# Optimization experiments

Hardware: AMD Instinct MI355X
Metric: run time of the kernel (lower is better)

The kernel has to match this reference:

```python
import jax, jax.numpy as jnp
import numpy as np

DROPOUT_RATE = 0.6


def dropout(x, key, rate=DROPOUT_RATE):
    keep = jax.random.bernoulli(key, 1.0 - rate, x.shape)
    return jnp.where(keep, x / (1.0 - rate), 0.0).astype(x.dtype)


def gcn_conv(x, W, b, src, dst, n_nodes):
    # h = x @ W  (tiny linear), then symmetric-normalized scatter-add over edges
    h = x @ W                                             # [N, C_out]
    deg = jax.ops.segment_sum(jnp.ones_like(dst, dtype=h.dtype), dst,
                              num_segments=n_nodes)       # in-degree at targets
    dinv = jnp.where(deg > 0, jax.lax.rsqrt(jnp.maximum(deg, 1.0)), 0.0)
    norm = dinv[src] * dinv[dst]                          # [E]
    msg = h[src] * norm[:, None]                          # [E, C_out] gather
    out = jax.ops.segment_sum(msg, dst, num_segments=n_nodes)  # scatter-add
    return out + b


def setup_inputs() -> dict:
    key = jax.random.key(0)
    k_x, k_e, k_w1, k_w2 = jax.random.split(key, 4)
    N, E = 100000, 6400000
    x = jax.random.normal(k_x, (N, 1), dtype=jnp.float32)
    edge_index = jax.random.randint(k_e, (2, E), 0, N, dtype=jnp.int64)
    # GCNConv weights (glorot-ish scale) and zero biases
    W1 = jax.random.normal(k_w1, (1, 16), dtype=jnp.float32) * (1.0 / np.sqrt(1.0))
    b1 = jnp.zeros((16,), dtype=jnp.float32)
    W2 = jax.random.normal(k_w2, (16, 1), dtype=jnp.float32) * (1.0 / np.sqrt(16.0))
    b2 = jnp.zeros((1,), dtype=jnp.float32)
    return {"x": x, "edge_index": edge_index, "W1": W1, "b1": b1, "W2": W2, "b2": b2}


def reference(x, edge_index, W1, b1, W2, b2):
    n_nodes = x.shape[0]
    src, dst = edge_index[0], edge_index[1]
    k1, k2 = jax.random.split(jax.random.key(42), 2)
    h = dropout(x, k1)
    h = gcn_conv(h, W1, b1, src, dst, n_nodes)
    h = jax.nn.relu(h)
    h = dropout(h, k2)
    out = gcn_conv(h, W2, b2, src, dst, n_nodes)
    return out
```

## Files before the change

### kernel.cpp

```cpp
#include <hip/hip_runtime.h>
#include <hip/hip_bf16.h>
#include <stdint.h>


#define KEEP_P 0.4f
#define RANGE 2048
#define SHIFT 11
#define MASK 2047
#define BPC 512
#define KS 32
#define SEGS (BPC / KS)
#define NBMAX 64
#define TILE 2048
#define TILE4 (TILE / 4)

__host__ __device__ inline unsigned rotl32(unsigned v, int s) {
  return (v << s) | (v >> (32 - s));
}

__host__ __device__ inline void threefry2x32(unsigned key0, unsigned key1,
                                             unsigned x0, unsigned x1,
                                             unsigned& o0, unsigned& o1) {
  unsigned ks0 = key0, ks1 = key1, ks2 = key0 ^ key1 ^ 0x1BD11BDAu;
  unsigned v0 = x0 + ks0, v1 = x1 + ks1;
#define TF_R(r) { v0 += v1; v1 = rotl32(v1, r); v1 ^= v0; }
  TF_R(13) TF_R(15) TF_R(26) TF_R(6)
  v0 += ks1; v1 += ks2 + 1u;
  TF_R(17) TF_R(29) TF_R(16) TF_R(24)
  v0 += ks2; v1 += ks0 + 2u;
  TF_R(13) TF_R(15) TF_R(26) TF_R(6)
  v0 += ks0; v1 += ks1 + 3u;
  TF_R(17) TF_R(29) TF_R(16) TF_R(24)
  v0 += ks1; v1 += ks2 + 4u;
  TF_R(13) TF_R(15) TF_R(26) TF_R(6)
  v0 += ks2; v1 += ks0 + 5u;
#undef TF_R
  o0 = v0; o1 = v1;
}

__device__ inline float u01_from_bits(unsigned bits) {
  return __uint_as_float((bits >> 9) | 0x3f800000u) - 1.0f;
}

__global__ __launch_bounds__(256) void k_part(
    const int* __restrict__ src, const int* __restrict__ dst,
    unsigned* __restrict__ slots, unsigned* __restrict__ cnt,
    int NB, int CAP, int e4, int E) {
  __shared__ unsigned hist[NBMAX], scan_s[NBMAX + 1], off[NBMAX];
  __shared__ unsigned tbase[NBMAX], cur[NBMAX];
  __shared__ unsigned stage[TILE];
  __shared__ unsigned char stage_p[TILE];
  const int tid = threadIdx.x;
  const size_t blkbase = (size_t)blockIdx.x * NB;
  unsigned* myslots = slots + blkbase * CAP;
  for (int p = tid; p < NB; p += 256) cur[p] = (unsigned)(p * CAP);
  const int chunk = (e4 + BPC - 1) / BPC;
  const int j0 = blockIdx.x * chunk;
  const int j1 = min(j0 + chunk, e4);
  const int4* dst4 = reinterpret_cast<const int4*>(dst);
  const int4* src4 = reinterpret_cast<const int4*>(src);

  for (int t0 = j0; t0 < j1; t0 += TILE4) {
    __syncthreads();
    for (int p = tid; p < NB; p += 256) hist[p] = 0u;
    __syncthreads();
    const int ja = t0 + tid, jb = t0 + TILE4 / 2 + tid;
    const bool va = ja < j1 && tid < TILE4 / 2;
    const bool vb = jb < j1;
    int4 da, db;
    if (va) {
      da = dst4[ja];
      atomicAdd(&hist[(unsigned)da.x >> SHIFT], 1u);
      atomicAdd(&hist[(unsigned)da.y >> SHIFT], 1u);
      atomicAdd(&hist[(unsigned)da.z >> SHIFT], 1u);
      atomicAdd(&hist[(unsigned)da.w >> SHIFT], 1u);
    }
    if (vb) {
      db = dst4[jb];
      atomicAdd(&hist[(unsigned)db.x >> SHIFT], 1u);
      atomicAdd(&hist[(unsigned)db.y >> SHIFT], 1u);
      atomicAdd(&hist[(unsigned)db.z >> SHIFT], 1u);
      atomicAdd(&hist[(unsigned)db.w >> SHIFT], 1u);
    }
    __syncthreads();
    if (tid == 0) {
      unsigned acc = 0;
      for (int p = 0; p < NB; ++p) { scan_s[p] = acc; acc += hist[p]; }
      scan_s[NB] = acc;
    }
    __syncthreads();
    for (int p = tid; p < NB; p += 256) {
      off[p] = scan_s[p];
      tbase[p] = cur[p];
      cur[p] += hist[p];
    }
    __syncthreads();
#define STAGE1(d, s) { unsigned ud = (unsigned)(d), us = (unsigned)(s); \
    unsigned p = ud >> SHIFT; unsigned pos = atomicAdd(&off[p], 1u); \
    stage[pos] = (ud & MASK) | (us << SHIFT); stage_p[pos] = (unsigned char)p; }
    if (va) {
      int4 sa = src4[ja];
      STAGE1(da.x, sa.x) STAGE1(da.y, sa.y) STAGE1(da.z, sa.z) STAGE1(da.w, sa.w)
    }
    if (vb) {
      int4 sb = src4[jb];
      STAGE1(db.x, sb.x) STAGE1(db.y, sb.y) STAGE1(db.z, sb.z) STAGE1(db.w, sb.w)
    }
#undef STAGE1
    __syncthreads();
    const int tc = (int)scan_s[NB];
    for (int i = tid; i < tc; i += 256) {
      unsigned p = stage_p[i];
      myslots[tbase[p] + ((unsigned)i - scan_s[p])] = stage[i];
    }
  }
  __syncthreads();
  if (blockIdx.x == 0) {
    for (int t = e4 * 4 + tid; t < E; t += 256) {
      unsigned ud = (unsigned)dst[t], us = (unsigned)src[t];
      unsigned p = ud >> SHIFT;
      unsigned pos = atomicAdd(&cur[p], 1u);
      myslots[pos] = (ud & MASK) | (us << SHIFT);
    }
  }
  __syncthreads();
  for (int p = tid; p < NB; p += 256)
    cnt[blkbase + p] = cur[p] - (unsigned)(p * CAP);
}

__global__ __launch_bounds__(256) void k_deg2(
    const unsigned* __restrict__ slots, const unsigned* __restrict__ cnt,
    unsigned short* __restrict__ part16, int NB, int CAP) {
  __shared__ unsigned bins[RANGE / 2];
  const int tid = threadIdx.x, w = tid >> 6, lane = tid & 63;
  const int p = blockIdx.y, kd = blockIdx.x;
  for (int i = tid; i < RANGE / 2; i += 256) bins[i] = 0u;
  __syncthreads();
  const int b0 = kd * SEGS + w;
  int l[4]; const unsigned* e[4];
#pragma unroll
  for (int s = 0; s < 4; ++s) {
    const int b = b0 + 4 * s;
    l[s] = cnt[(size_t)b * NB + p];
    e[s] = slots + ((size_t)b * NB + p) * CAP;
  }
  const int base1 = 4 * lane, base2 = base1 + 256;
  uint4 u[8]; bool f[8];
#pragma unroll
  for (int s = 0; s < 4; ++s) {
    f[2 * s]     = base1 + 4 <= l[s];
    f[2 * s + 1] = base2 + 4 <= l[s];
    if (f[2 * s])     u[2 * s]     = *reinterpret_cast<const uint4*>(e[s] + base1);
    if (f[2 * s + 1]) u[2 * s + 1] = *reinterpret_cast<const uint4*>(e[s] + base2);
  }
#define DEG_ONE(v) { unsigned r = (v) & MASK; \
    atomicAdd(&bins[r >> 1], 1u << ((r & 1) * 16)); }
#pragma unroll
  for (int j = 0; j < 8; ++j) {
    if (f[j]) { DEG_ONE(u[j].x) DEG_ONE(u[j].y) DEG_ONE(u[j].z) DEG_ONE(u[j].w) }
  }
#pragma unroll
  for (int s = 0; s < 4; ++s) {
    if (!f[2 * s])     for (int k = base1; k < l[s]; ++k) DEG_ONE(e[s][k])
    if (!f[2 * s + 1]) for (int k = base2; k < l[s]; ++k) DEG_ONE(e[s][k])
  }
#undef DEG_ONE
  __syncthreads();
  unsigned* my32 = (unsigned*)(part16 + ((size_t)kd * gridDim.y + p) * RANGE);
  for (int i = tid; i < RANGE / 2; i += 256) my32[i] = bins[i];
}

__global__ __launch_bounds__(256) void k_node1(
    const float* __restrict__ x, const unsigned short* __restrict__ part16,
    float* __restrict__ dinv, float* __restrict__ y,
    int NB, int n, unsigned k1a, unsigned k1b) {
  int i = blockIdx.x * blockDim.x + threadIdx.x;
  if (i >= n) return;
  const int p = i >> SHIFT, r = i & MASK;
  unsigned d = 0;
  for (int b = 0; b < KS; ++b)
    d += part16[((size_t)b * NB + p) * RANGE + r];
  float di = (d > 0) ? (1.0f / sqrtf((float)d)) : 0.0f;
  dinv[i] = di;
  unsigned o0, o1;
  threefry2x32(k1a, k1b, 0u, (unsigned)i, o0, o1);
  float u = u01_from_bits(o0 ^ o1);
  float xd = (u < KEEP_P) ? (x[i] / KEEP_P) : 0.0f;
  y[i] = xd * di;
}

__global__ __launch_bounds__(256) void k_scat(
    const unsigned* __restrict__ slots, const unsigned* __restrict__ cnt,
    const float* __restrict__ val, float* __restrict__ part,
    int NB, int CAP) {
  __shared__ float bins[RANGE];
  const int tid = threadIdx.x, w = tid >> 6, lane = tid & 63;
  const int p = blockIdx.y, ks = blockIdx.x;
  for (int i = tid; i < RANGE; i += 256) bins[i] = 0.0f;
  __syncthreads();
  const int b0 = ks * SEGS + w;
  int l[4]; const unsigned* e[4];
#pragma unroll
  for (int s = 0; s < 4; ++s) {
    const int b = b0 + 4 * s;
    l[s] = cnt[(size_t)b * NB + p];
    e[s] = slots + ((size_t)b * NB + p) * CAP;
  }
  const int base1 = 4 * lane, base2 = base1 + 256;
  uint4 u[8]; bool f[8];
#pragma unroll
  for (int s = 0; s < 4; ++s) {
    f[2 * s]     = base1 + 4 <= l[s];
    f[2 * s + 1] = base2 + 4 <= l[s];
    if (f[2 * s])     u[2 * s]     = *reinterpret_cast<const uint4*>(e[s] + base1);
    if (f[2 * s + 1]) u[2 * s + 1] = *reinterpret_cast<const uint4*>(e[s] + base2);
  }
  float g[32];
#pragma unroll
  for (int j = 0; j < 8; ++j) {
    if (f[j]) {
      g[4 * j]     = val[u[j].x >> SHIFT];
      g[4 * j + 1] = val[u[j].y >> SHIFT];
      g[4 * j + 2] = val[u[j].z >> SHIFT];
      g[4 * j + 3] = val[u[j].w >> SHIFT];
    }
  }
#pragma unroll
  for (int j = 0; j < 8; ++j) {
    if (f[j]) {
      atomicAdd(&bins[u[j].x & MASK], g[4 * j]);
      atomicAdd(&bins[u[j].y & MASK], g[4 * j + 1]);
      atomicAdd(&bins[u[j].z & MASK], g[4 * j + 2]);
      atomicAdd(&bins[u[j].w & MASK], g[4 * j + 3]);
    }
  }
#pragma unroll
  for (int s = 0; s < 4; ++s) {
    if (!f[2 * s]) {
      for (int k = base1; k < l[s]; ++k) {
        unsigned v = e[s][k];
        atomicAdd(&bins[v & MASK], val[v >> SHIFT]);
      }
    }
    if (!f[2 * s + 1]) {
      for (int k = base2; k < l[s]; ++k) {
        unsigned v = e[s][k];
        atomicAdd(&bins[v & MASK], val[v >> SHIFT]);
      }
    }
  }
  __syncthreads();
  float* my = part + ((size_t)ks * NB + p) * RANGE;
  for (int i = tid; i < RANGE; i += 256) my[i] = bins[i];
}

__global__ __launch_bounds__(256) void k_node2(
    const float* __restrict__ part, const float* __restrict__ dinv,
    const float* __restrict__ W1, const float* __restrict__ b1,
    const float* __restrict__ W2, float* __restrict__ z2,
    int NB, int n, unsigned k2a, unsigned k2b) {
  int i = blockIdx.x * blockDim.x + threadIdx.x;
  if (i >= n) return;
  const int p = i >> SHIFT, r = i & MASK;
  float s = 0.0f;
  for (int b = 0; b < KS; ++b)
    s += part[((size_t)b * NB + p) * RANGE + r];
  float t = s * dinv[i];
  float z = 0.0f;
  unsigned base = (unsigned)i * 16u;
#pragma unroll
  for (int c = 0; c < 16; ++c) {
    float h = W1[c] * t + b1[c];
    h = fmaxf(h, 0.0f);
    unsigned o0, o1;
    threefry2x32(k2a, k2b, 0u, base + (unsigned)c, o0, o1);
    float u = u01_from_bits(o0 ^ o1);
    float hd = (u < KEEP_P) ? (h / KEEP_P) : 0.0f;
    z += hd * W2[c];
  }
  z2[i] = z * dinv[i];
}

__global__ __launch_bounds__(256) void k_final(
    const float* __restrict__ part, const float* __restrict__ dinv,
    const float* __restrict__ b2, float* __restrict__ out,
    int NB, int n) {
  int i = blockIdx.x * blockDim.x + threadIdx.x;
  if (i >= n) return;
  const int p = i >> SHIFT, r = i & MASK;
  float s = 0.0f;
  for (int b = 0; b < KS; ++b)
    s += part[((size_t)b * NB + p) * RANGE + r];
  out[i] = b2[0] + dinv[i] * s;
}

extern "C" void kernel_launch(void* const* d_in, const int* in_sizes, int n_in,
                              void* d_out, int out_size, void* d_ws, size_t ws_size,
                              hipStream_t stream) {
  const float* x  = (const float*)d_in[0];
  const int* edge = (const int*)d_in[1];
  const float* W1 = (const float*)d_in[2];
  const float* b1 = (const float*)d_in[3];
  const float* W2 = (const float*)d_in[4];
  const float* b2 = (const float*)d_in[5];
  float* out = (float*)d_out;

  const int N = in_sizes[0];
  const int E = in_sizes[1] / 2;
  const int* src = edge;
  const int* dst = edge + E;

  const int NP = (N + 255) & ~255;
  const int NB = (N + RANGE - 1) / RANGE;

  const size_t cnt_sz  = (size_t)BPC * NB * 4;
  const size_t part_sz = (size_t)KS * NB * RANGE * 4;
  const size_t small_sz = (size_t)3 * NP * 4;
  size_t fixed = cnt_sz + part_sz + small_sz + 512;
  size_t avail = ws_size > fixed ? ws_size - fixed : 0;
  int CAP = (int)(avail / ((size_t)NB * BPC * 4));
  CAP &= ~3;
  if (CAP > 512) CAP = 512;
  if (CAP < 288) CAP = 288;

  char* w = (char*)d_ws;
  unsigned* slots = (unsigned*)w;        w += (size_t)NB * BPC * CAP * 4;
  unsigned* cnt   = (unsigned*)w;        w += cnt_sz;
  w = (char*)(((uintptr_t)w + 255) & ~(uintptr_t)255);
  float* part_f = (float*)w;
  unsigned short* part16 = (unsigned short*)w;
  w += part_sz;
  float* dinv = (float*)w;
  float* y    = dinv + NP;
  float* z2   = y + NP;

  unsigned k1a, k1b, k2a, k2b;
  threefry2x32(0u, 42u, 0u, 0u, k1a, k1b);
  threefry2x32(0u, 42u, 0u, 1u, k2a, k2b);

  const int e4 = E >> 2;
  const int gN = (N + 255) / 256;

  k_part <<<BPC, 256, 0, stream>>>(src, dst, slots, cnt, NB, CAP, e4, E);
  k_deg2 <<<dim3(KS, NB), 256, 0, stream>>>(slots, cnt, part16, NB, CAP);
  k_node1<<<gN, 256, 0, stream>>>(x, part16, dinv, y, NB, N, k1a, k1b);
  k_scat <<<dim3(KS, NB), 256, 0, stream>>>(slots, cnt, y, part_f, NB, CAP);
  k_node2<<<gN, 256, 0, stream>>>(part_f, dinv, W1, b1, W2, z2, NB, N, k2a, k2b);
  k_scat <<<dim3(KS, NB), 256, 0, stream>>>(slots, cnt, z2, part_f, NB, CAP);
  k_final<<<gN, 256, 0, stream>>>(part_f, dinv, b2, out, NB, N);
}
```

Before: 245.8 us.

## Double edge-bucket count and split wavefronts across two segments per pass

Raises the number of binning blocks (BPC) from 512 to 1024, which shrinks per-bucket capacity (CAP clamp 176–208). The degree and scatter kernels now give each wavefront SEGS/4 segments, with the two half-waves handling different segments using 32 lanes × 2 uint4 loads. Tail handling moves from per-lane scalar loops to a single lane per segment. The aim is a more even load with less wasted slot padding, at the cost of more segments per block and a risk of bucket overflow if the smaller capacity is exceeded.

```diff
diff --git a/kernel.cpp b/kernel.cpp
--- a/kernel.cpp
+++ b/kernel.cpp
@@ -7,9 +7,10 @@
 #define RANGE 2048
 #define SHIFT 11
 #define MASK 2047
-#define BPC 512
+#define BPC 1024
 #define KS 32
 #define SEGS (BPC / KS)
+#define SPW (SEGS / 4)
 #define NBMAX 64
 #define TILE 2048
 #define TILE4 (TILE / 4)
@@ -136,33 +137,32 @@
   const int p = blockIdx.y, kd = blockIdx.x;
   for (int i = tid; i < RANGE / 2; i += 256) bins[i] = 0u;
   __syncthreads();
-  const int b0 = kd * SEGS + w;
-  int l[4]; const unsigned* e[4];
-#pragma unroll
-  for (int s = 0; s < 4; ++s) {
-    const int b = b0 + 4 * s;
+  int l[SPW]; const unsigned* e[SPW];
+#pragma unroll
+  for (int s = 0; s < SPW; ++s) {
+    const int b = kd * SEGS + w * SPW + s;
     l[s] = cnt[(size_t)b * NB + p];
     e[s] = slots + ((size_t)b * NB + p) * CAP;
   }
-  const int base1 = 4 * lane, base2 = base1 + 256;
-  uint4 u[8]; bool f[8];
-#pragma unroll
-  for (int s = 0; s < 4; ++s) {
-    f[2 * s]     = base1 + 4 <= l[s];
-    f[2 * s + 1] = base2 + 4 <= l[s];
-    if (f[2 * s])     u[2 * s]     = *reinterpret_cast<const uint4*>(e[s] + base1);
-    if (f[2 * s + 1]) u[2 * s + 1] = *reinterpret_cast<const uint4*>(e[s] + base2);
-  }
+  const int half = lane >> 5, li = lane & 31;
 #define DEG_ONE(v) { unsigned r = (v) & MASK; \
     atomicAdd(&bins[r >> 1], 1u << ((r & 1) * 16)); }
 #pragma unroll
-  for (int j = 0; j < 8; ++j) {
-    if (f[j]) { DEG_ONE(u[j].x) DEG_ONE(u[j].y) DEG_ONE(u[j].z) DEG_ONE(u[j].w) }
-  }
-#pragma unroll
-  for (int s = 0; s < 4; ++s) {
-    if (!f[2 * s])     for (int k = base1; k < l[s]; ++k) DEG_ONE(e[s][k])
-    if (!f[2 * s + 1]) for (int k = base2; k < l[s]; ++k) DEG_ONE(e[s][k])
+  for (int r = 0; r < SPW / 2; ++r) {
+    const int s = 2 * r + half;
+    const unsigned* es = e[s];
+    const int ls = l[s];
+    const int i1 = 4 * li, i2 = 128 + 4 * li;
+    const bool f1 = i1 + 4 <= ls, f2 = i2 + 4 <= ls;
+    uint4 u1, u2;
+    if (f1) u1 = *reinterpret_cast<const uint4*>(es + i1);
+    if (f2) u2 = *reinterpret_cast<const uint4*>(es + i2);
+    if (f1) { DEG_ONE(u1.x) DEG_ONE(u1.y) DEG_ONE(u1.z) DEG_ONE(u1.w) }
+    if (f2) { DEG_ONE(u2.x) DEG_ONE(u2.y) DEG_ONE(u2.z) DEG_ONE(u2.w) }
+  }
+  if (lane < SPW) {
+    const int s = lane;
+    for (int k = l[s] & ~3; k < l[s]; ++k) DEG_ONE(e[s][k])
   }
 #undef DEG_ONE
   __syncthreads();
@@ -198,55 +198,51 @@
   const int p = blockIdx.y, ks = blockIdx.x;
   for (int i = tid; i < RANGE; i += 256) bins[i] = 0.0f;
   __syncthreads();
-  const int b0 = ks * SEGS + w;
-  int l[4]; const unsigned* e[4];
-#pragma unroll
-  for (int s = 0; s < 4; ++s) {
-    const int b = b0 + 4 * s;
+  int l[SPW]; const unsigned* e[SPW];
+#pragma unroll
+  for (int s = 0; s < SPW; ++s) {
+    const int b = ks * SEGS + w * SPW + s;
     l[s] = cnt[(size_t)b * NB + p];
     e[s] = slots + ((size_t)b * NB + p) * CAP;
   }
-  const int base1 = 4 * lane, base2 = base1 + 256;
-  uint4 u[8]; bool f[8];
-#pragma unroll
-  for (int s = 0; s < 4; ++s) {
-    f[2 * s]     = base1 + 4 <= l[s];
-    f[2 * s + 1] = base2 + 4 <= l[s];
-    if (f[2 * s])     u[2 * s]     = *reinterpret_cast<const uint4*>(e[s] + base1);
-    if (f[2 * s + 1]) u[2 * s + 1] = *reinterpret_cast<const uint4*>(e[s] + base2);
-  }
-  float g[32];
-#pragma unroll
-  for (int j = 0; j < 8; ++j) {
-    if (f[j]) {
-      g[4 * j]     = val[u[j].x >> SHIFT];
-      g[4 * j + 1] = val[u[j].y >> SHIFT];
-      g[4 * j + 2] = val[u[j].z >> SHIFT];
-      g[4 * j + 3] = val[u[j].w >> SHIFT];
-    }
-  }
-#pragma unroll
-  for (int j = 0; j < 8; ++j) {
-    if (f[j]) {
-      atomicAdd(&bins[u[j].x & MASK], g[4 * j]);
-      atomicAdd(&bins[u[j].y & MASK], g[4 * j + 1]);
-      atomicAdd(&bins[u[j].z & MASK], g[4 * j + 2]);
-      atomicAdd(&bins[u[j].w & MASK], g[4 * j + 3]);
-    }
-  }
-#pragma unroll
-  for (int s = 0; s < 4; ++s) {
-    if (!f[2 * s]) {
-      for (int k = base1; k < l[s]; ++k) {
-        unsigned v = e[s][k];
-        atomicAdd(&bins[v & MASK], val[v >> SHIFT]);
-      }
-    }
-    if (!f[2 * s + 1]) {
-      for (int k = base2; k < l[s]; ++k) {
-        unsigned v = e[s][k];
-        atomicAdd(&bins[v & MASK], val[v >> SHIFT]);
-      }
+  const int half = lane >> 5, li = lane & 31;
+#pragma unroll
+  for (int r = 0; r < SPW / 2; ++r) {
+    const int s = 2 * r + half;
+    const unsigned* es = e[s];
+    const int ls = l[s];
+    const int i1 = 4 * li, i2 = 128 + 4 * li;
+    const bool f1 = i1 + 4 <= ls, f2 = i2 + 4 <= ls;
+    uint4 u1, u2;
+    if (f1) u1 = *reinterpret_cast<const uint4*>(es + i1);
+    if (f2) u2 = *reinterpret_cast<const uint4*>(es + i2);
+    float g0, g1, g2, g3, g4, g5, g6, g7;
+    if (f1) {
+      g0 = val[u1.x >> SHIFT]; g1 = val[u1.y >> SHIFT];
+      g2 = val[u1.z >> SHIFT]; g3 = val[u1.w >> SHIFT];
+    }
+    if (f2) {
+      g4 = val[u2.x >> SHIFT]; g5 = val[u2.y >> SHIFT];
+      g6 = val[u2.z >> SHIFT]; g7 = val[u2.w >> SHIFT];
+    }
+    if (f1) {
+      atomicAdd(&bins[u1.x & MASK], g0);
+      atomicAdd(&bins[u1.y & MASK], g1);
+      atomicAdd(&bins[u1.z & MASK], g2);
+      atomicAdd(&bins[u1.w & MASK], g3);
+    }
+    if (f2) {
+      atomicAdd(&bins[u2.x & MASK], g4);
+      atomicAdd(&bins[u2.y & MASK], g5);
+      atomicAdd(&bins[u2.z & MASK], g6);
+      atomicAdd(&bins[u2.w & MASK], g7);
+    }
+  }
+  if (lane < SPW) {
+    const int s = lane;
+    for (int k = l[s] & ~3; k < l[s]; ++k) {
+      unsigned v = e[s][k];
+      atomicAdd(&bins[v & MASK], val[v >> SHIFT]);
     }
   }
   __syncthreads();
@@ -320,8 +316,8 @@
   size_t avail = ws_size > fixed ? ws_size - fixed : 0;
   int CAP = (int)(avail / ((size_t)NB * BPC * 4));
   CAP &= ~3;
-  if (CAP > 512) CAP = 512;
-  if (CAP < 288) CAP = 288;
+  if (CAP > 208) CAP = 208;
+  if (CAP < 176) CAP = 176;
 
   char* w = (char*)d_ws;
   unsigned* slots = (unsigned*)w;        w += (size_t)NB * BPC * CAP * 4;
```

Result: faster. 223.4 us (-9.1%).
